# Kernel optimization log

Measured on AMD Instinct MI355X. Metric: run time of the kernel, lower is better.

## Reference

```python
import jax, jax.numpy as jnp
import numpy as np

N_NODES = 100000
N_EDGES = 50000
NNZ = 1600000
C = 128
EPS = 0.0  # train_eps=False -> fixed buffer


def setup_inputs() -> dict:
    key = jax.random.key(0)
    k0, k1, k2, k3, k4 = jax.random.split(key, 5)
    x_0 = jax.random.normal(k0, (N_NODES, C), dtype=jnp.float32)
    node_idx = jax.random.randint(k1, (NNZ,), 0, N_NODES, dtype=jnp.int64)
    edge_idx = jax.random.randint(k2, (NNZ,), 0, N_EDGES, dtype=jnp.int64)
    # Linear(in_channels, in_channels) params (kaiming-uniform-ish scale)
    lim = 1.0 / np.sqrt(C)
    W = jax.random.uniform(k3, (C, C), minval=-lim, maxval=lim, dtype=jnp.float32)
    b = jax.random.uniform(k4, (C,), minval=-lim, maxval=lim, dtype=jnp.float32)
    return {"x_0": x_0, "node_idx": node_idx, "edge_idx": edge_idx, "W": W, "b": b}


def reference(x_0, node_idx, edge_idx, W, b):
    # Step 1: x_1 = B_1^T @ x_0  (hyperedge e sums features of its nodes)
    x_1 = jax.ops.segment_sum(x_0[node_idx], edge_idx, num_segments=N_EDGES)
    # Step 2: m_{1->0} = B_1 @ x_1 (node sums features of its incident hyperedges)
    m_1_0 = jax.ops.segment_sum(x_1[edge_idx], node_idx, num_segments=N_NODES)
    # Step 3: GIN update: Theta @ ((1+eps)*x_0 + m)
    out_0 = ((1.0 + EPS) * x_0 + m_1_0) @ W.T + b
    return (out_0, x_1)
```

## Files before the change

### kernel.cpp

```cpp
#include <hip/hip_runtime.h>
#include <stdint.h>

#define N_NODES 100000
#define N_EDGES 50000
#define C 128
#define NB 196
#define CAP 12288
#define X0_BLOCKS 25000

typedef short short8 __attribute__((ext_vector_type(8)));
typedef float f32x4  __attribute__((ext_vector_type(4)));

__device__ __forceinline__ unsigned int bf16rne(float f) {
    unsigned int u = __float_as_uint(f);
    return (u + 0x7FFFu + ((u >> 16) & 1u)) >> 16;
}
__device__ __forceinline__ unsigned int pk_bf16(float x, float y) {
    return (bf16rne(y) << 16) | bf16rne(x);
}
__device__ __forceinline__ float bf_lo(unsigned int u) { return __uint_as_float(u << 16); }
__device__ __forceinline__ float bf_hi(unsigned int u) { return __uint_as_float(u & 0xFFFF0000u); }

__global__ __launch_bounds__(256) void conv_all(
    const float2* __restrict__ x0, const float2* __restrict__ W,
    unsigned int* __restrict__ x0h, unsigned int* __restrict__ Whu,
    int* __restrict__ CehCnh)
{
    int bid = blockIdx.x, t = threadIdx.x;
    if (bid < X0_BLOCKS) {
        int i = bid * 256 + t;
        float2 v = x0[i];
        x0h[i] = pk_bf16(v.x, v.y);
        if (bid == 0)
            for (int k = t; k < 2 * NB; k += 256) CehCnh[k] = 0;
    } else {
        int i = (bid - X0_BLOCKS) * 256 + t;
        float2 v = W[i];
        Whu[i] = pk_bf16(v.x, v.y);
    }
}

__global__ __launch_bounds__(256) void coarse_hist(
    const int* __restrict__ nidx, const int* __restrict__ eidx,
    int* __restrict__ Ceh, int* __restrict__ Cnh, int nnz)
{
    __shared__ int he[NB], hn[NB];
    int t = threadIdx.x;
    int chunk0 = blockIdx.x * 4096;
    for (int k = t; k < NB; k += 256) { he[k] = 0; hn[k] = 0; }
    __syncthreads();
#pragma unroll 4
    for (int j = 0; j < 16; ++j) {
        int i = chunk0 + j * 256 + t;
        if (i < nnz) {
            atomicAdd(&he[eidx[i] >> 8], 1);
            atomicAdd(&hn[nidx[i] >> 9], 1);
        }
    }
    __syncthreads();
    for (int k = t; k < NB; k += 256) {
        if (he[k]) atomicAdd(&Ceh[k], he[k]);
        if (hn[k]) atomicAdd(&Cnh[k], hn[k]);
    }
}

__global__ __launch_bounds__(256) void coarse_scan(
    const int* __restrict__ Ceh, const int* __restrict__ Cnh,
    int* __restrict__ Cecur, int* __restrict__ Cncur)
{
    __shared__ int s[256];
    int t = threadIdx.x;
    int v = (t < NB) ? Ceh[t] : 0;
    s[t] = v; __syncthreads();
    for (int d = 1; d < 256; d <<= 1) {
        int u = (t >= d) ? s[t - d] : 0;
        __syncthreads(); s[t] += u; __syncthreads();
    }
    if (t < NB) Cecur[t] = s[t] - v;
    __syncthreads();
    v = (t < NB) ? Cnh[t] : 0;
    s[t] = v; __syncthreads();
    for (int d = 1; d < 256; d <<= 1) {
        int u = (t >= d) ? s[t - d] : 0;
        __syncthreads(); s[t] += u; __syncthreads();
    }
    if (t < NB) Cncur[t] = s[t] - v;
}

__global__ __launch_bounds__(256) void partition_kernel(
    const int* __restrict__ nidx, const int* __restrict__ eidx,
    int* __restrict__ Cecur, int* __restrict__ Cncur,
    unsigned int* __restrict__ pe, unsigned int* __restrict__ pn, int nnz)
{
    __shared__ int he[NB], hn[NB], be[NB], bn[NB];
    int t = threadIdx.x;
    int chunk0 = blockIdx.x * 4096;
    for (int k = t; k < NB; k += 256) { he[k] = 0; hn[k] = 0; }
    __syncthreads();
#pragma unroll 4
    for (int j = 0; j < 16; ++j) {
        int i = chunk0 + j * 256 + t;
        if (i < nnz) {
            atomicAdd(&he[eidx[i] >> 8], 1);
            atomicAdd(&hn[nidx[i] >> 9], 1);
        }
    }
    __syncthreads();
    for (int k = t; k < NB; k += 256) {
        be[k] = atomicAdd(&Cecur[k], he[k]);
        bn[k] = atomicAdd(&Cncur[k], hn[k]);
        he[k] = 0; hn[k] = 0;
    }
    __syncthreads();
#pragma unroll 4
    for (int j = 0; j < 16; ++j) {
        int i = chunk0 + j * 256 + t;
        if (i < nnz) {
            int e = eidx[i], n = nidx[i];
            int re = atomicAdd(&he[e >> 8], 1);
            pe[be[e >> 8] + re] = (unsigned int)((e & 255) | (n << 8));
            int rn = atomicAdd(&hn[n >> 9], 1);
            pn[bn[n >> 9] + rn] = (unsigned int)((n & 511) | (e << 9));
        }
    }
}

__global__ __launch_bounds__(256) void bucket_scatter_ex(
    const unsigned int* __restrict__ pe, const unsigned int* __restrict__ pn,
    const int* __restrict__ Cecur, const int* __restrict__ Cncur,
    int* __restrict__ e_list, int* __restrict__ n_list,
    int* __restrict__ eoff, int* __restrict__ noff)
{
    __shared__ int cnt[512], cur[512], s[256];
    __shared__ int vals[CAP];
    bool eside = blockIdx.x < NB;
    int b = eside ? blockIdx.x : blockIdx.x - NB;
    const unsigned int* pairs = eside ? pe : pn;
    const int* endarr         = eside ? Cecur : Cncur;
    int* out                  = eside ? e_list : n_list;
    int* off                  = eside ? eoff : noff;
    int shift = eside ? 8 : 9;
    int mask  = (1 << shift) - 1;
    int kpb   = 1 << shift;
    int nkeys = eside ? N_EDGES : N_NODES;
    int key0 = b * kpb;
    int nk = nkeys - key0; if (nk > kpb) nk = kpb;
    if (nk <= 0) return;
    int start = (b == 0) ? 0 : endarr[b - 1];
    int end   = endarr[b];
    int t = threadIdx.x;

    for (int k = t; k < nk; k += 256) cnt[k] = 0;
    __syncthreads();
    for (int i = start + t; i < end; i += 256)
        atomicAdd(&cnt[(int)(pairs[i] & mask)], 1);
    __syncthreads();
    int k0 = 2 * t, k1 = 2 * t + 1;
    int c0 = (k0 < nk) ? cnt[k0] : 0;
    int c1 = (k1 < nk) ? cnt[k1] : 0;
    int local = c0 + c1;
    s[t] = local; __syncthreads();
    for (int d = 1; d < 256; d <<= 1) {
        int u = (t >= d) ? s[t - d] : 0;
        __syncthreads(); s[t] += u; __syncthreads();
    }
    int excl = s[t] - local;
    if (k0 < nk) { cur[k0] = excl;      off[key0 + k0] = start + excl; }
    if (k1 < nk) { cur[k1] = excl + c0; off[key0 + k1] = start + excl + c0; }
    if (b == NB - 1 && t == 0) off[nkeys] = end;
    __syncthreads();
    for (int i = start + t; i < end; i += 256) {
        unsigned int p = pairs[i];
        int key = (int)(p & mask);
        int val = (int)(p >> shift);
        int pos = atomicAdd(&cur[key], 1);
        if (pos < CAP) vals[pos] = val;
        else out[start + pos] = val;
    }
    __syncthreads();
    int sz = end - start; if (sz > CAP) sz = CAP;
    for (int j = t; j < sz; j += 256) out[start + j] = vals[j];
}

__device__ __forceinline__ float2 gather_bf16_rows(
    const unsigned int* __restrict__ src, const int* __restrict__ list,
    int s0, int s1, int lane)
{
    float ax0=0,ay0=0,ax1=0,ay1=0,ax2=0,ay2=0,ax3=0,ay3=0;
    float ax4=0,ay4=0,ax5=0,ay5=0,ax6=0,ay6=0,ax7=0,ay7=0;
    for (int base = s0; base < s1; base += 64) {
        int cnt = s1 - base; if (cnt > 64) cnt = 64;
        int my = (lane < cnt) ? list[base + lane] : 0;
        int j = 0;
        for (; j + 8 <= cnt; j += 8) {
            int g0 = __shfl(my, j+0), g1 = __shfl(my, j+1);
            int g2 = __shfl(my, j+2), g3 = __shfl(my, j+3);
            int g4 = __shfl(my, j+4), g5 = __shfl(my, j+5);
            int g6 = __shfl(my, j+6), g7 = __shfl(my, j+7);
            unsigned int u0 = src[(size_t)g0 * 64 + lane];
            unsigned int u1 = src[(size_t)g1 * 64 + lane];
            unsigned int u2 = src[(size_t)g2 * 64 + lane];
            unsigned int u3 = src[(size_t)g3 * 64 + lane];
            unsigned int u4 = src[(size_t)g4 * 64 + lane];
            unsigned int u5 = src[(size_t)g5 * 64 + lane];
            unsigned int u6 = src[(size_t)g6 * 64 + lane];
            unsigned int u7 = src[(size_t)g7 * 64 + lane];
            ax0 += bf_lo(u0); ay0 += bf_hi(u0);  ax1 += bf_lo(u1); ay1 += bf_hi(u1);
            ax2 += bf_lo(u2); ay2 += bf_hi(u2);  ax3 += bf_lo(u3); ay3 += bf_hi(u3);
            ax4 += bf_lo(u4); ay4 += bf_hi(u4);  ax5 += bf_lo(u5); ay5 += bf_hi(u5);
            ax6 += bf_lo(u6); ay6 += bf_hi(u6);  ax7 += bf_lo(u7); ay7 += bf_hi(u7);
        }
        for (; j < cnt; ++j) {
            int g = __shfl(my, j);
            unsigned int u = src[(size_t)g * 64 + lane];
            ax0 += bf_lo(u); ay0 += bf_hi(u);
        }
    }
    ax0+=ax1; ay0+=ay1; ax2+=ax3; ay2+=ay3; ax4+=ax5; ay4+=ay5; ax6+=ax7; ay6+=ay7;
    ax0+=ax2; ay0+=ay2; ax4+=ax6; ay4+=ay6;
    ax0+=ax4; ay0+=ay4;
    return make_float2(ax0, ay0);
}

__global__ __launch_bounds__(256) void seg_sum(
    const unsigned int* __restrict__ x0h, const int* __restrict__ list,
    const int* __restrict__ off, float2* __restrict__ x1,
    unsigned int* __restrict__ x1h, int nseg)
{
    int wid  = (blockIdx.x * 256 + threadIdx.x) >> 6;
    int lane = threadIdx.x & 63;
    if (wid >= nseg) return;
    float2 acc = gather_bf16_rows(x0h, list, off[wid], off[wid + 1], lane);
    x1 [(size_t)wid * 64 + lane] = acc;
    x1h[(size_t)wid * 64 + lane] = pk_bf16(acc.x, acc.y);
}

__global__ __launch_bounds__(256) void gin_fused(
    const unsigned int* __restrict__ x0h, const unsigned int* __restrict__ x1h,
    const int* __restrict__ n_list, const int* __restrict__ noff,
    const unsigned short* __restrict__ Wh, const float* __restrict__ b,
    float* __restrict__ out)
{
    __shared__ __align__(16) unsigned short ins[32][136];
    int t = threadIdx.x;
    int lane = t & 63, w = t >> 6;
    int row0 = blockIdx.x * 32;

    for (int r = w * 8; r < w * 8 + 8; ++r) {
        int node = row0 + r;
        unsigned int bu = x0h[(size_t)node * 64 + lane];
        float2 g = gather_bf16_rows(x1h, n_list, noff[node], noff[node + 1], lane);
        g.x += bf_lo(bu); g.y += bf_hi(bu);
        *(unsigned int*)&ins[r][lane * 2] = pk_bf16(g.x, g.y);
    }
    __syncthreads();

    int mt  = w & 1;
    int ntb = (w >> 1) * 4;
    int l15  = lane & 15;
    int koff = (lane >> 4) * 8;
    int arow = mt * 16 + l15;

    f32x4 acc0 = {0,0,0,0}, acc1 = {0,0,0,0}, acc2 = {0,0,0,0}, acc3 = {0,0,0,0};
#pragma unroll
    for (int kt = 0; kt < C; kt += 32) {
        short8 a = *(const short8*)&ins[arow][kt + koff];
        short8 b0 = *(const short8*)&Wh[(size_t)((ntb + 0) * 16 + l15) * C + kt + koff];
        short8 b1 = *(const short8*)&Wh[(size_t)((ntb + 1) * 16 + l15) * C + kt + koff];
        short8 b2 = *(const short8*)&Wh[(size_t)((ntb + 2) * 16 + l15) * C + kt + koff];
        short8 b3 = *(const short8*)&Wh[(size_t)((ntb + 3) * 16 + l15) * C + kt + koff];
        acc0 = __builtin_amdgcn_mfma_f32_16x16x32_bf16(a, b0, acc0, 0, 0, 0);
        acc1 = __builtin_amdgcn_mfma_f32_16x16x32_bf16(a, b1, acc1, 0, 0, 0);
        acc2 = __builtin_amdgcn_mfma_f32_16x16x32_bf16(a, b2, acc2, 0, 0, 0);
        acc3 = __builtin_amdgcn_mfma_f32_16x16x32_bf16(a, b3, acc3, 0, 0, 0);
    }

    int drow = row0 + mt * 16 + (lane >> 4) * 4;
#pragma unroll
    for (int n = 0; n < 4; ++n) {
        f32x4 accv = (n == 0) ? acc0 : (n == 1) ? acc1 : (n == 2) ? acc2 : acc3;
        int colg = (ntb + n) * 16 + l15;
        float bias = b[colg];
#pragma unroll
        for (int j = 0; j < 4; ++j)
            out[(size_t)(drow + j) * C + colg] = accv[j] + bias;
    }
}

__global__ __launch_bounds__(256) void scatter_rows(
    const float4* __restrict__ src, const int* __restrict__ gather_idx,
    const int* __restrict__ scatter_idx, float* __restrict__ dst, int nnz)
{
    int gid = blockIdx.x * 256 + threadIdx.x;
    int row = gid >> 5, lane = gid & 31;
    if (row >= nnz) return;
    float4 v = src[(size_t)gather_idx[row] * 32 + lane];
    float* d = dst + (size_t)scatter_idx[row] * C + lane * 4;
    atomicAdd(d + 0, v.x); atomicAdd(d + 1, v.y);
    atomicAdd(d + 2, v.z); atomicAdd(d + 3, v.w);
}

__global__ __launch_bounds__(256) void gin_gemm(
    const float* __restrict__ x0, const float* __restrict__ m,
    const float* __restrict__ W, const float* __restrict__ b,
    float* __restrict__ out)
{
    __shared__ float Ws[32][129];
    __shared__ float insf[32][33];
    int t = threadIdx.x;
    int col = t & 127, rg = t >> 7;
    int row0 = blockIdx.x * 32;
    float acc[16];
#pragma unroll
    for (int r = 0; r < 16; ++r) acc[r] = 0.f;
    float bias = b[col];
    for (int kt = 0; kt < C; kt += 32) {
#pragma unroll
        for (int j = 0; j < 16; ++j) {
            int i = j * 256 + t, wc = i >> 5, kl = i & 31;
            Ws[kl][wc] = W[(size_t)wc * C + kt + kl];
        }
#pragma unroll
        for (int j = 0; j < 4; ++j) {
            int i = j * 256 + t, r = i >> 5, kl = i & 31;
            size_t gi = (size_t)(row0 + r) * C + kt + kl;
            insf[r][kl] = x0[gi] + m[gi];
        }
        __syncthreads();
#pragma unroll
        for (int kl = 0; kl < 32; ++kl) {
            float wv = Ws[kl][col];
#pragma unroll
            for (int r = 0; r < 16; ++r)
                acc[r] += insf[rg * 16 + r][kl] * wv;
        }
        __syncthreads();
    }
#pragma unroll
    for (int r = 0; r < 16; ++r)
        out[(size_t)(row0 + rg * 16 + r) * C + col] = acc[r] + bias;
}

extern "C" void kernel_launch(void* const* d_in, const int* in_sizes, int n_in,
                              void* d_out, int out_size, void* d_ws, size_t ws_size,
                              hipStream_t stream) {
    const float* x0 = (const float*)d_in[0];
    const int* nidx = (const int*)d_in[1];
    const int* eidx = (const int*)d_in[2];
    const float* W  = (const float*)d_in[3];
    const float* b  = (const float*)d_in[4];

    float* out0 = (float*)d_out;
    float* x1   = out0 + (size_t)N_NODES * C;
    int nnz = in_sizes[1];

    auto align64 = [](char* q) {
        return (char*)(((uintptr_t)q + 63) & ~(uintptr_t)63);
    };
    char* p = (char*)d_ws;
    unsigned int* pe = (unsigned int*)p; p = align64(p + (size_t)nnz * 4);
    unsigned int* pn = (unsigned int*)p; p = align64(p + (size_t)nnz * 4);
    unsigned int* x0h = (unsigned int*)p; p = align64(p + (size_t)N_NODES * 64 * 4);
    int* e_list = (int*)p; p = align64(p + (size_t)nnz * 4);
    int* n_list = (int*)p; p = align64(p + (size_t)nnz * 4);
    int* eoff   = (int*)p; p = align64(p + (size_t)(N_EDGES + 1) * 4);
    int* noff   = (int*)p; p = align64(p + (size_t)(N_NODES + 1) * 4);
    int* Ceh    = (int*)p;
    int* Cnh    = Ceh + NB;
    p = align64((char*)(Cnh + NB));
    int* Cecur  = (int*)p; p = align64(p + NB * 4);
    int* Cncur  = (int*)p; p = align64(p + NB * 4);
    unsigned int* x1h = (unsigned int*)p; p = align64(p + (size_t)N_EDGES * 64 * 4);
    unsigned int* Whu = (unsigned int*)p; p = align64(p + (size_t)C * C / 2 * 4);
    size_t needed = (size_t)(p - (char*)d_ws);

    if (ws_size < needed) {
        float* m = (float*)d_ws;
        hipMemsetAsync(x1, 0, (size_t)N_EDGES * C * sizeof(float), stream);
        hipMemsetAsync(m,  0, (size_t)N_NODES * C * sizeof(float), stream);
        int blocks = (nnz + 7) / 8;
        scatter_rows<<<blocks, 256, 0, stream>>>((const float4*)x0, nidx, eidx, x1, nnz);
        scatter_rows<<<blocks, 256, 0, stream>>>((const float4*)x1, eidx, nidx, m, nnz);
        gin_gemm<<<N_NODES / 32, 256, 0, stream>>>(x0, m, W, b, out0);
        return;
    }

    int pblocks = (nnz + 4095) / 4096;

    conv_all<<<X0_BLOCKS + C * C / 2 / 256, 256, 0, stream>>>(
        (const float2*)x0, (const float2*)W, x0h, Whu, Ceh);

    coarse_hist<<<pblocks, 256, 0, stream>>>(nidx, eidx, Ceh, Cnh, nnz);
    coarse_scan<<<1, 256, 0, stream>>>(Ceh, Cnh, Cecur, Cncur);
    partition_kernel<<<pblocks, 256, 0, stream>>>(
        nidx, eidx, Cecur, Cncur, pe, pn, nnz);
    bucket_scatter_ex<<<2 * NB, 256, 0, stream>>>(
        pe, pn, Cecur, Cncur, e_list, n_list, eoff, noff);

    seg_sum<<<(N_EDGES * 64 + 255) / 256, 256, 0, stream>>>(
        x0h, e_list, eoff, (float2*)x1, x1h, N_EDGES);

    gin_fused<<<N_NODES / 32, 256, 0, stream>>>(
        x0h, x1h, n_list, noff,
        (const unsigned short*)Whu, b, out0);
}
```

Before: 248.5 us.

## Fuse histogram, scan and partition into one cooperative kernel

Replaces the three front-end CSR kernels (coarse histogram, single-block scan, partition) with one cooperative kernel that uses grid-wide syncs. Indices are held in registers between phases, so they are read once, and two launch boundaries disappear. The workspace layout also moves to 256-byte alignment with x1h placed next to x0h. The non-cooperative path stays as a fallback if the cooperative launch fails. Grid syncs cost something of their own, and all blocks must be co-resident.

```diff
diff --git a/kernel.cpp b/kernel.cpp
--- a/kernel.cpp
+++ b/kernel.cpp
@@ -1,5 +1,8 @@
 #include <hip/hip_runtime.h>
+#include <hip/hip_cooperative_groups.h>
 #include <stdint.h>
+
+namespace cg = cooperative_groups;
 
 #define N_NODES 100000
 #define N_EDGES 50000
@@ -37,6 +40,78 @@
         int i = (bid - X0_BLOCKS) * 256 + t;
         float2 v = W[i];
         Whu[i] = pk_bf16(v.x, v.y);
+    }
+}
+
+__global__ __launch_bounds__(256) void csr_front(
+    const int* __restrict__ nidx, const int* __restrict__ eidx,
+    int* __restrict__ Ceh, int* __restrict__ Cnh,
+    int* __restrict__ Cecur, int* __restrict__ Cncur,
+    unsigned int* __restrict__ pe, unsigned int* __restrict__ pn, int nnz)
+{
+    cg::grid_group grid = cg::this_grid();
+    __shared__ int he[NB], hn[NB], be[NB], bn[NB];
+    __shared__ int s[256];
+    int t = threadIdx.x;
+    int chunk0 = blockIdx.x * 4096;
+
+    int ev[16], nv[16];
+#pragma unroll
+    for (int j = 0; j < 16; ++j) {
+        int i = chunk0 + j * 256 + t;
+        ev[j] = (i < nnz) ? eidx[i] : -1;
+        nv[j] = (i < nnz) ? nidx[i] : -1;
+    }
+    for (int k = t; k < NB; k += 256) { he[k] = 0; hn[k] = 0; }
+    __syncthreads();
+#pragma unroll
+    for (int j = 0; j < 16; ++j) {
+        if (ev[j] >= 0) {
+            atomicAdd(&he[ev[j] >> 8], 1);
+            atomicAdd(&hn[nv[j] >> 9], 1);
+        }
+    }
+    __syncthreads();
+    for (int k = t; k < NB; k += 256) {
+        if (he[k]) atomicAdd(&Ceh[k], he[k]);
+        if (hn[k]) atomicAdd(&Cnh[k], hn[k]);
+    }
+    grid.sync();
+
+    if (blockIdx.x == 0) {
+        int v = (t < NB) ? Ceh[t] : 0;
+        s[t] = v; __syncthreads();
+        for (int d = 1; d < 256; d <<= 1) {
+            int u = (t >= d) ? s[t - d] : 0;
+            __syncthreads(); s[t] += u; __syncthreads();
+        }
+        if (t < NB) Cecur[t] = s[t] - v;
+        __syncthreads();
+        v = (t < NB) ? Cnh[t] : 0;
+        s[t] = v; __syncthreads();
+        for (int d = 1; d < 256; d <<= 1) {
+            int u = (t >= d) ? s[t - d] : 0;
+            __syncthreads(); s[t] += u; __syncthreads();
+        }
+        if (t < NB) Cncur[t] = s[t] - v;
+    }
+    grid.sync();
+
+    for (int k = t; k < NB; k += 256) {
+        be[k] = he[k] ? atomicAdd(&Cecur[k], he[k]) : 0;
+        bn[k] = hn[k] ? atomicAdd(&Cncur[k], hn[k]) : 0;
+        he[k] = 0; hn[k] = 0;
+    }
+    __syncthreads();
+#pragma unroll
+    for (int j = 0; j < 16; ++j) {
+        if (ev[j] >= 0) {
+            int e = ev[j], n = nv[j];
+            int re = atomicAdd(&he[e >> 8], 1);
+            pe[be[e >> 8] + re] = (unsigned int)((e & 255) | (n << 8));
+            int rn = atomicAdd(&hn[n >> 9], 1);
+            pn[bn[n >> 9] + rn] = (unsigned int)((n & 511) | (e << 9));
+        }
     }
 }
 
@@ -354,24 +429,24 @@
     float* x1   = out0 + (size_t)N_NODES * C;
     int nnz = in_sizes[1];
 
-    auto align64 = [](char* q) {
-        return (char*)(((uintptr_t)q + 63) & ~(uintptr_t)63);
+    auto align256 = [](char* q) {
+        return (char*)(((uintptr_t)q + 255) & ~(uintptr_t)255);
     };
-    char* p = (char*)d_ws;
-    unsigned int* pe = (unsigned int*)p; p = align64(p + (size_t)nnz * 4);
-    unsigned int* pn = (unsigned int*)p; p = align64(p + (size_t)nnz * 4);
-    unsigned int* x0h = (unsigned int*)p; p = align64(p + (size_t)N_NODES * 64 * 4);
-    int* e_list = (int*)p; p = align64(p + (size_t)nnz * 4);
-    int* n_list = (int*)p; p = align64(p + (size_t)nnz * 4);
-    int* eoff   = (int*)p; p = align64(p + (size_t)(N_EDGES + 1) * 4);
-    int* noff   = (int*)p; p = align64(p + (size_t)(N_NODES + 1) * 4);
+    char* p = align256((char*)d_ws);
+    unsigned int* pe = (unsigned int*)p; p = align256(p + (size_t)nnz * 4);
+    unsigned int* pn = (unsigned int*)p; p = align256(p + (size_t)nnz * 4);
+    unsigned int* x0h = (unsigned int*)p; p = align256(p + (size_t)N_NODES * 64 * 4);
+    unsigned int* x1h = (unsigned int*)p; p = align256(p + (size_t)N_EDGES * 64 * 4);
+    int* e_list = (int*)p; p = align256(p + (size_t)nnz * 4);
+    int* n_list = (int*)p; p = align256(p + (size_t)nnz * 4);
+    int* eoff   = (int*)p; p = align256(p + (size_t)(N_EDGES + 1) * 4);
+    int* noff   = (int*)p; p = align256(p + (size_t)(N_NODES + 1) * 4);
     int* Ceh    = (int*)p;
     int* Cnh    = Ceh + NB;
-    p = align64((char*)(Cnh + NB));
-    int* Cecur  = (int*)p; p = align64(p + NB * 4);
-    int* Cncur  = (int*)p; p = align64(p + NB * 4);
-    unsigned int* x1h = (unsigned int*)p; p = align64(p + (size_t)N_EDGES * 64 * 4);
-    unsigned int* Whu = (unsigned int*)p; p = align64(p + (size_t)C * C / 2 * 4);
+    p = align256((char*)(Cnh + NB));
+    int* Cecur  = (int*)p; p = align256(p + NB * 4);
+    int* Cncur  = (int*)p; p = align256(p + NB * 4);
+    unsigned int* Whu = (unsigned int*)p; p = align256(p + (size_t)C * C / 2 * 4);
     size_t needed = (size_t)(p - (char*)d_ws);
 
     if (ws_size < needed) {
@@ -390,10 +465,20 @@
     conv_all<<<X0_BLOCKS + C * C / 2 / 256, 256, 0, stream>>>(
         (const float2*)x0, (const float2*)W, x0h, Whu, Ceh);
 
-    coarse_hist<<<pblocks, 256, 0, stream>>>(nidx, eidx, Ceh, Cnh, nnz);
-    coarse_scan<<<1, 256, 0, stream>>>(Ceh, Cnh, Cecur, Cncur);
-    partition_kernel<<<pblocks, 256, 0, stream>>>(
-        nidx, eidx, Cecur, Cncur, pe, pn, nnz);
+    {
+        void* args[] = { (void*)&nidx, (void*)&eidx, (void*)&Ceh, (void*)&Cnh,
+                         (void*)&Cecur, (void*)&Cncur, (void*)&pe, (void*)&pn,
+                         (void*)&nnz };
+        hipError_t err = hipLaunchCooperativeKernel(
+            (const void*)csr_front, dim3(pblocks), dim3(256), args, 0, stream);
+        if (err != hipSuccess) {
+            coarse_hist<<<pblocks, 256, 0, stream>>>(nidx, eidx, Ceh, Cnh, nnz);
+            coarse_scan<<<1, 256, 0, stream>>>(Ceh, Cnh, Cecur, Cncur);
+            partition_kernel<<<pblocks, 256, 0, stream>>>(
+                nidx, eidx, Cecur, Cncur, pe, pn, nnz);
+        }
+    }
+
     bucket_scatter_ex<<<2 * NB, 256, 0, stream>>>(
         pe, pn, Cecur, Cncur, e_list, n_list, eoff, noff);
 
```

Result: slower. 315.4 us (+26.9%).
